# Kernel optimization log

Hardware: AMD Instinct MI355X
Metric: run time of the kernel (lower is better)

The kernel has to match this reference:

```python
import jax, jax.numpy as jnp
import numpy as np

N_ATOMS = 50000
N_EDGES = 1_600_000
N_MOL = 500
HIDDEN = 128
FILTERS = 128
GAUSS = 50
LAYERS = 3
CUTOFF = 10.0
LOG2 = 0.6931471805599453


def ssp(x):
    # ShiftedSoftplus: softplus(x) - log(2)
    return jax.nn.softplus(x) - LOG2


def setup_inputs() -> dict:
    key = jax.random.key(0)
    ks = jax.random.split(key, 24)
    z = jax.random.randint(ks[0], (N_ATOMS,), 0, 100)
    pos = jax.random.uniform(ks[1], (N_ATOMS, 3), jnp.float32) * 5.0  # box keeps d < cutoff
    batch = jnp.sort(jax.random.randint(ks[2], (N_ATOMS,), 0, N_MOL))
    row = jax.random.randint(ks[3], (N_EDGES,), 0, N_ATOMS)
    off = jax.random.randint(ks[4], (N_EDGES,), 1, N_ATOMS)
    col = (row + off) % N_ATOMS  # guarantees row != col (no zero distances)
    edge_index = jnp.stack([row, col])
    def lin(k, fi, fo):
        return jax.random.normal(k, (fi, fo), jnp.float32) * (1.0 / np.sqrt(fi))
    emb = jax.random.normal(ks[5], (100, HIDDEN), jnp.float32)
    mlp1_w = jnp.stack([lin(jax.random.fold_in(ks[6], i), GAUSS, FILTERS) for i in range(LAYERS)])
    mlp1_b = jnp.zeros((LAYERS, FILTERS), jnp.float32)
    mlp2_w = jnp.stack([lin(jax.random.fold_in(ks[7], i), FILTERS, FILTERS) for i in range(LAYERS)])
    mlp2_b = jnp.zeros((LAYERS, FILTERS), jnp.float32)
    lin1_w = jnp.stack([lin(jax.random.fold_in(ks[8], i), HIDDEN, FILTERS) for i in range(LAYERS)])
    lin2_w = jnp.stack([lin(jax.random.fold_in(ks[9], i), FILTERS, HIDDEN) for i in range(LAYERS)])
    lin2_b = jnp.zeros((LAYERS, HIDDEN), jnp.float32)
    int_w = jnp.stack([lin(jax.random.fold_in(ks[10], i), HIDDEN, HIDDEN) for i in range(LAYERS)])
    int_b = jnp.zeros((LAYERS, HIDDEN), jnp.float32)
    out1_w = lin(ks[11], HIDDEN, HIDDEN // 2)
    out1_b = jnp.zeros((HIDDEN // 2,), jnp.float32)
    out2_w = lin(ks[12], HIDDEN // 2, 1)
    out2_b = jnp.zeros((1,), jnp.float32)
    return {"z": z, "pos": pos, "batch": batch, "edge_index": edge_index,
            "emb": emb, "mlp1_w": mlp1_w, "mlp1_b": mlp1_b, "mlp2_w": mlp2_w, "mlp2_b": mlp2_b,
            "lin1_w": lin1_w, "lin2_w": lin2_w, "lin2_b": lin2_b, "int_w": int_w, "int_b": int_b,
            "out1_w": out1_w, "out1_b": out1_b, "out2_w": out2_w, "out2_b": out2_b}


def reference(z, pos, batch, edge_index, emb, mlp1_w, mlp1_b, mlp2_w, mlp2_b,
              lin1_w, lin2_w, lin2_b, int_w, int_b, out1_w, out1_b, out2_w, out2_b):
    row, col = edge_index[0], edge_index[1]  # source j, target i
    d = jnp.linalg.norm(pos[row] - pos[col], axis=-1)  # [E]
    # GaussianSmearing
    offset = jnp.linspace(0.0, CUTOFF, GAUSS)
    coeff = -0.5 / (offset[1] - offset[0]) ** 2
    rbf = jnp.exp(coeff * (d[:, None] - offset[None, :]) ** 2)  # [E, GAUSS]
    # cosine cutoff
    C = 0.5 * (jnp.cos(d * jnp.pi / CUTOFF) + 1.0)  # [E]
    h = emb[z]  # [N, H]
    for l in range(LAYERS):
        W = ssp(rbf @ mlp1_w[l] + mlp1_b[l]) @ mlp2_w[l] + mlp2_b[l]  # [E, F]
        W = W * C[:, None]
        x = h @ lin1_w[l]                 # [N, F]
        msg = x[row] * W                  # gather from source, per-edge filter
        agg = jax.ops.segment_sum(msg, col, num_segments=N_ATOMS)  # scatter-add to targets
        x = agg @ lin2_w[l] + lin2_b[l]
        x = ssp(x)
        x = x @ int_w[l] + int_b[l]
        h = h + x                         # residual
    h = ssp(h @ out1_w + out1_b)
    h = h @ out2_w + out2_b               # [N, 1] per-atom energy
    out = jax.ops.segment_sum(h[:, 0], batch, num_segments=N_MOL)  # 'add' readout
    return out.reshape(-1)
```

## Files before the change

### kernel.cpp

```cpp
#include <hip/hip_runtime.h>
#include <math.h>

#define HID 128
#define NGAUSS 50
#define TBL 2048
#define TBL2 8192
#define DMAX 8.6605f
#define LDX 136
#define PGRID 768

typedef _Float16 h4 __attribute__((ext_vector_type(4)));
typedef _Float16 f16x8 __attribute__((ext_vector_type(8)));
typedef float f32x4 __attribute__((ext_vector_type(4)));

__device__ __forceinline__ float sspf(float x) {
  float ax = fabsf(x);
  return fmaxf(x, 0.0f) + log1pf(expf(-ax)) - 0.69314718055994530942f;
}

__global__ __launch_bounds__(128) void build_table_k(
    const float* __restrict__ w1, const float* __restrict__ b1,
    const float* __restrict__ w2, const float* __restrict__ b2,
    float* __restrict__ tab) {
  int l = blockIdx.x >> 11;
  int ti = blockIdx.x & (TBL - 1);
  int j = threadIdx.x;
  __shared__ float rbf[NGAUSS];
  __shared__ float v1[HID];
  const float step = DMAX / (float)(TBL - 1);
  float d = ti * step;
  if (j < NGAUSS) {
    const float gstep = 10.0f / 49.0f;
    const float gcoeff = -12.005f;
    float diff = d - j * gstep;
    rbf[j] = expf(gcoeff * diff * diff);
  }
  __syncthreads();
  float s = b1[l * HID + j];
  const float* w1p = w1 + l * NGAUSS * HID + j;
  for (int g = 0; g < NGAUSS; g++) s = fmaf(rbf[g], w1p[g * HID], s);
  v1[j] = sspf(s);
  __syncthreads();
  float s2 = b2[l * HID + j];
  const float* w2p = w2 + l * HID * HID + j;
  for (int k = 0; k < HID; k++) s2 = fmaf(v1[k], w2p[k * HID], s2);
  float C = 0.5f * (cosf(d * 0.3141592653589793f) + 1.0f);
  tab[((size_t)l * TBL + ti) * HID + j] = s2 * C;
}

__global__ __launch_bounds__(256) void upsample_k(
    const float* __restrict__ tab, _Float16* __restrict__ tabh) {
  int idx = blockIdx.x * 256 + threadIdx.x;
  if (idx >= 3 * TBL2 * HID) return;
  int ch = idx & 127;
  int i = (idx >> 7) & (TBL2 - 1);
  int l = idx >> 20;
  float t = (float)i * ((float)(TBL - 1) / (float)(TBL2 - 1));
  int i0 = min((int)t, TBL - 2);
  float f = t - (float)i0;
  const float* base = tab + ((size_t)l * TBL + i0) * HID + ch;
  tabh[idx] = (_Float16)fmaf(f, base[HID] - base[0], base[0]);
}

__global__ __launch_bounds__(256) void wswz10_k(
    const float* __restrict__ lin1, const float* __restrict__ lin2,
    const float* __restrict__ intw, const float* __restrict__ out1w,
    _Float16* __restrict__ out) {
  int b = blockIdx.x;
  int t = threadIdx.x;
  if (b < 9) {
    const float* src = (b < 3 ? lin1 : (b < 6 ? lin2 : intw)) + (size_t)(b % 3) * HID * HID;
    _Float16* dst = out + (size_t)b * 16384;
    for (int i = t; i < 16384; i += 256) {
      int j = i & 7;
      int lane = (i >> 3) & 63;
      int kk = (i >> 9) & 3;
      int ntc = i >> 11;
      int n = ntc * 16 + (lane & 15);
      int k = kk * 32 + (lane >> 4) * 8 + j;
      dst[i] = (_Float16)src[k * HID + n];
    }
  } else {
    _Float16* dst = out + (size_t)9 * 16384;
    for (int i = t; i < 8192; i += 256) {
      int j = i & 7;
      int lane = (i >> 3) & 63;
      int kk = (i >> 9) & 3;
      int ntc = i >> 11;
      int n = ntc * 16 + (lane & 15);
      int k = kk * 32 + (lane >> 4) * 8 + j;
      dst[i] = (_Float16)out1w[k * 64 + n];
    }
  }
}

__global__ __launch_bounds__(256) void emb_gather_k(
    const int* __restrict__ z, const float* __restrict__ emb,
    _Float16* __restrict__ h16, int N) {
  int i4 = blockIdx.x * 256 + threadIdx.x;
  if (i4 >= N * 32) return;
  int a = i4 >> 5;
  float4 v = ((const float4*)emb)[z[a] * 32 + (i4 & 31)];
  h4 o;
  o.x = (_Float16)v.x; o.y = (_Float16)v.y;
  o.z = (_Float16)v.z; o.w = (_Float16)v.w;
  ((h4*)h16)[i4] = o;
}

__global__ __launch_bounds__(256) void bcount_k(
    const int* __restrict__ col, int* __restrict__ bcount, int E, int nbuck) {
  __shared__ int hist[1024];
  int t = threadIdx.x;
  int e0 = blockIdx.x * 2048;
  for (int j = t; j < nbuck; j += 256) hist[j] = 0;
  __syncthreads();
#pragma unroll
  for (int u = 0; u < 8; u++) {
    int e = e0 + u * 256 + t;
    if (e < E) atomicAdd(&hist[col[e] >> 6], 1);
  }
  __syncthreads();
  for (int j = t; j < nbuck; j += 256)
    if (hist[j]) atomicAdd(&bcount[j], hist[j]);
}

__global__ __launch_bounds__(256) void bucket_scan_k(
    const int* __restrict__ bcount, int* __restrict__ bstart,
    int* __restrict__ bcur, int nbuck, int* __restrict__ starts, int N) {
  __shared__ int sh[256];
  int t = threadIdx.x;
  int chunk = (nbuck + 255) / 256;
  int b0 = t * chunk;
  int c[8];
  int s = 0;
  for (int j = 0; j < chunk; j++) {
    int idx = b0 + j;
    int v = (idx < nbuck) ? bcount[idx] : 0;
    c[j] = v;
    s += v;
  }
  sh[t] = s;
  __syncthreads();
  for (int o = 1; o < 256; o <<= 1) {
    int v = (t >= o) ? sh[t - o] : 0;
    __syncthreads();
    sh[t] += v;
    __syncthreads();
  }
  int p = (t == 0) ? 0 : sh[t - 1];
  for (int j = 0; j < chunk; j++) {
    int idx = b0 + j;
    if (idx < nbuck) {
      bstart[idx] = p;
      bcur[idx] = p;
      p += c[j];
    }
  }
  if (t == 255) {
    bstart[nbuck] = p;
    starts[N] = p;
  }
}

__global__ __launch_bounds__(256) void scatterA_k(
    const int* __restrict__ row, const int* __restrict__ col,
    const float* __restrict__ pos, int* __restrict__ bcur,
    unsigned long long* __restrict__ tmp, int E, int nbuck) {
  __shared__ int hist[1024];
  __shared__ int base[1024];
  int t = threadIdx.x;
  int e0 = blockIdx.x * 2048;
  for (int j = t; j < nbuck; j += 256) hist[j] = 0;
  __syncthreads();
  int bkt[8];
  int rnk[8];
  unsigned long long key[8];
#pragma unroll
  for (int u = 0; u < 8; u++) {
    int e = e0 + u * 256 + t;
    bkt[u] = -1;
    if (e < E) {
      int r = row[e], c = col[e];
      float dx = pos[r * 3 + 0] - pos[c * 3 + 0];
      float dy = pos[r * 3 + 1] - pos[c * 3 + 1];
      float dz = pos[r * 3 + 2] - pos[c * 3 + 2];
      float d = sqrtf(dx * dx + dy * dy + dz * dz);
      const float inv2 = (float)(TBL2 - 1) / DMAX;
      int q = min((int)(d * inv2 + 0.5f), TBL2 - 1);
      unsigned int pay = ((unsigned int)r << 13) | (unsigned int)q;
      key[u] = ((unsigned long long)pay << 6) | (unsigned long long)(c & 63);
      bkt[u] = c >> 6;
      rnk[u] = atomicAdd(&hist[bkt[u]], 1);
    }
  }
  __syncthreads();
  for (int j = t; j < nbuck; j += 256)
    base[j] = hist[j] ? atomicAdd(&bcur[j], hist[j]) : 0;
  __syncthreads();
#pragma unroll
  for (int u = 0; u < 8; u++)
    if (bkt[u] >= 0) tmp[(size_t)base[bkt[u]] + rnk[u]] = key[u];
}

__global__ __launch_bounds__(256) void scatterB_k(
    const unsigned long long* __restrict__ tmp, const int* __restrict__ bstart,
    int* __restrict__ starts, unsigned int* __restrict__ payload, int N) {
  int j = blockIdx.x;
  int t = threadIdx.x;
  __shared__ int cnt[64];
  __shared__ int cur[64];
  int rs = bstart[j], re = bstart[j + 1];
  if (t < 64) cnt[t] = 0;
  __syncthreads();
  for (int e = rs + t; e < re; e += 256)
    atomicAdd(&cnt[(int)(tmp[e] & 63)], 1);
  __syncthreads();
  if (t < 64) {
    int mine = cnt[t];
    int v = mine;
    for (int o = 1; o < 64; o <<= 1) {
      int u = __shfl_up(v, o, 64);
      if (t >= o) v += u;
    }
    int excl = v - mine;
    int c = j * 64 + t;
    if (c < N) starts[c] = rs + excl;
    cur[t] = rs + excl;
  }
  __syncthreads();
  for (int e = rs + t; e < re; e += 256) {
    unsigned long long k = tmp[e];
    int p = atomicAdd(&cur[(int)(k & 63)], 1);
    payload[p] = (unsigned int)(k >> 6);
  }
}


__global__ __launch_bounds__(256, 4) void lin_p_k(
    const _Float16* __restrict__ in16, const _Float16* __restrict__ Wg,
    _Float16* __restrict__ out16, int N, int ntiles) {
  __shared__ __align__(16) _Float16 Xs[32 * LDX];
  __shared__ __align__(16) _Float16 Ys[32 * LDX];
  int t = threadIdx.x;
  int lane = t & 63, w = t >> 6;
  int g = w & 1, c = w >> 1;
  int mrow = lane & 15, quad = lane >> 4;
  f32x4 zero = {0.f, 0.f, 0.f, 0.f};
  for (int tile = blockIdx.x; tile < ntiles; tile += gridDim.x) {
    int a0 = tile * 32;
#pragma unroll
    for (int p = 0; p < 2; p++) {
      int id = t + p * 256;
      int a = id >> 4, kg = id & 15;
      uint4 v = make_uint4(0, 0, 0, 0);
      if (a0 + a < N) v = ((const uint4*)in16)[(size_t)(a0 + a) * 16 + kg];
      *(uint4*)&Xs[a * LDX + kg * 8] = v;
    }
    __syncthreads();
    f16x8 af[4];
#pragma unroll
    for (int kk = 0; kk < 4; kk++)
      af[kk] = *(const f16x8*)&Xs[(g * 16 + mrow) * LDX + kk * 32 + quad * 8];
    f32x4 acc[4];
#pragma unroll
    for (int i = 0; i < 4; i++) acc[i] = zero;
#pragma unroll
    for (int kk = 0; kk < 4; kk++) {
#pragma unroll
      for (int nt = 0; nt < 4; nt++) {
        f16x8 bf = *(const f16x8*)(Wg + ((((c * 4 + nt) * 4 + kk) << 9) + lane * 8));
        acc[nt] = __builtin_amdgcn_mfma_f32_16x16x32_f16(af[kk], bf, acc[nt], 0, 0, 0);
      }
    }
#pragma unroll
    for (int nt = 0; nt < 4; nt++) {
      int colv = c * 64 + nt * 16 + mrow;
#pragma unroll
      for (int r = 0; r < 4; r++)
        Ys[(g * 16 + quad * 4 + r) * LDX + colv] = (_Float16)acc[nt][r];
    }
    __syncthreads();
#pragma unroll
    for (int p = 0; p < 2; p++) {
      int id = t + p * 256;
      int a = id >> 4, kg = id & 15;
      if (a0 + a < N)
        ((uint4*)out16)[(size_t)(a0 + a) * 16 + kg] = *(uint4*)&Ys[a * LDX + kg * 8];
    }
  }
}

__global__ __launch_bounds__(256, 4) void ssp_p_k(
    const _Float16* __restrict__ agg16, const _Float16* __restrict__ Wg,
    const float* __restrict__ bias, _Float16* __restrict__ y16, int N, int ntiles) {
  __shared__ __align__(16) _Float16 Xs[32 * LDX];
  __shared__ __align__(16) _Float16 Ys[32 * LDX];
  int t = threadIdx.x;
  int lane = t & 63, w = t >> 6;
  int g = w & 1, c = w >> 1;
  int mrow = lane & 15, quad = lane >> 4;
  float br[4];
#pragma unroll
  for (int nt = 0; nt < 4; nt++) br[nt] = bias[c * 64 + nt * 16 + mrow];
  f32x4 zero = {0.f, 0.f, 0.f, 0.f};
  for (int tile = blockIdx.x; tile < ntiles; tile += gridDim.x) {
    int a0 = tile * 32;
#pragma unroll
    for (int p = 0; p < 2; p++) {
      int id = t + p * 256;
      int a = id >> 4, kg = id & 15;
      uint4 v = make_uint4(0, 0, 0, 0);
      if (a0 + a < N) v = ((const uint4*)agg16)[(size_t)(a0 + a) * 16 + kg];
      *(uint4*)&Xs[a * LDX + kg * 8] = v;
    }
    __syncthreads();
    f16x8 af[4];
#pragma unroll
    for (int kk = 0; kk < 4; kk++)
      af[kk] = *(const f16x8*)&Xs[(g * 16 + mrow) * LDX + kk * 32 + quad * 8];
    f32x4 acc[4];
#pragma unroll
    for (int i = 0; i < 4; i++) acc[i] = zero;
#pragma unroll
    for (int kk = 0; kk < 4; kk++) {
#pragma unroll
      for (int nt = 0; nt < 4; nt++) {
        f16x8 bf = *(const f16x8*)(Wg + ((((c * 4 + nt) * 4 + kk) << 9) + lane * 8));
        acc[nt] = __builtin_amdgcn_mfma_f32_16x16x32_f16(af[kk], bf, acc[nt], 0, 0, 0);
      }
    }
#pragma unroll
    for (int nt = 0; nt < 4; nt++) {
      int colv = c * 64 + nt * 16 + mrow;
#pragma unroll
      for (int r = 0; r < 4; r++)
        Ys[(g * 16 + quad * 4 + r) * LDX + colv] = (_Float16)sspf(acc[nt][r] + br[nt]);
    }
    __syncthreads();
#pragma unroll
    for (int p = 0; p < 2; p++) {
      int id = t + p * 256;
      int a = id >> 4, kg = id & 15;
      if (a0 + a < N)
        ((uint4*)y16)[(size_t)(a0 + a) * 16 + kg] = *(uint4*)&Ys[a * LDX + kg * 8];
    }
  }
}

__global__ __launch_bounds__(256, 4) void res_p_k(
    const _Float16* __restrict__ y16, const _Float16* __restrict__ Wg,
    const float* __restrict__ bias, _Float16* __restrict__ h16, int N, int ntiles) {
  __shared__ __align__(16) _Float16 Xs[32 * LDX];
  __shared__ __align__(16) _Float16 Ys[32 * LDX];
  int t = threadIdx.x;
  int lane = t & 63, w = t >> 6;
  int g = w & 1, c = w >> 1;
  int mrow = lane & 15, quad = lane >> 4;
  float br[4];
#pragma unroll
  for (int nt = 0; nt < 4; nt++) br[nt] = bias[c * 64 + nt * 16 + mrow];
  f32x4 zero = {0.f, 0.f, 0.f, 0.f};
  for (int tile = blockIdx.x; tile < ntiles; tile += gridDim.x) {
    int a0 = tile * 32;
#pragma unroll
    for (int p = 0; p < 2; p++) {
      int id = t + p * 256;
      int a = id >> 4, kg = id & 15;
      uint4 v = make_uint4(0, 0, 0, 0);
      if (a0 + a < N) v = ((const uint4*)y16)[(size_t)(a0 + a) * 16 + kg];
      *(uint4*)&Xs[a * LDX + kg * 8] = v;
    }
    __syncthreads();
    f16x8 af[4];
#pragma unroll
    for (int kk = 0; kk < 4; kk++)
      af[kk] = *(const f16x8*)&Xs[(g * 16 + mrow) * LDX + kk * 32 + quad * 8];
    f32x4 acc[4];
#pragma unroll
    for (int i = 0; i < 4; i++) acc[i] = zero;
#pragma unroll
    for (int kk = 0; kk < 4; kk++) {
#pragma unroll
      for (int nt = 0; nt < 4; nt++) {
        f16x8 bf = *(const f16x8*)(Wg + ((((c * 4 + nt) * 4 + kk) << 9) + lane * 8));
        acc[nt] = __builtin_amdgcn_mfma_f32_16x16x32_f16(af[kk], bf, acc[nt], 0, 0, 0);
      }
    }
#pragma unroll
    for (int nt = 0; nt < 4; nt++) {
      int colv = c * 64 + nt * 16 + mrow;
#pragma unroll
      for (int r = 0; r < 4; r++)
        Ys[(g * 16 + quad * 4 + r) * LDX + colv] = (_Float16)(acc[nt][r] + br[nt]);
    }
    __syncthreads();
#pragma unroll
    for (int p = 0; p < 2; p++) {
      int id = t + p * 256;
      int a = id >> 4, kg = id & 15;
      if (a0 + a < N) {
        f16x8 hv = *(const f16x8*)&((const uint4*)h16)[(size_t)(a0 + a) * 16 + kg];
        f16x8 yv = *(f16x8*)&Ys[a * LDX + kg * 8];
        f16x8 o;
#pragma unroll
        for (int j = 0; j < 8; j++) o[j] = (_Float16)((float)hv[j] + (float)yv[j]);
        ((uint4*)h16)[(size_t)(a0 + a) * 16 + kg] = *(uint4*)&o;
      }
    }
  }
}

__global__ __launch_bounds__(256, 4) void energy_p_k(
    const _Float16* __restrict__ h16, const _Float16* __restrict__ Wg,
    const float* __restrict__ o1b, const float* __restrict__ o2w,
    const float* __restrict__ o2b, const int* __restrict__ batch,
    float* __restrict__ out, int N, int ntiles) {
  __shared__ __align__(16) _Float16 Xs[32 * LDX];
  __shared__ float ebuf[32];
  __shared__ int bat[32];
  int t = threadIdx.x;
  int lane = t & 63, w = t >> 6;
  int g = w & 1, c = w >> 1;
  int mrow = lane & 15, quad = lane >> 4;
  float br[2], wr[2];
#pragma unroll
  for (int nt = 0; nt < 2; nt++) {
    int colv = c * 32 + nt * 16 + mrow;
    br[nt] = o1b[colv];
    wr[nt] = o2w[colv];
  }
  float o2b0 = o2b[0];
  if (t < 32) ebuf[t] = 0.f;
  __syncthreads();
  f32x4 zero = {0.f, 0.f, 0.f, 0.f};
  for (int tile = blockIdx.x; tile < ntiles; tile += gridDim.x) {
    int a0 = tile * 32;
#pragma unroll
    for (int p = 0; p < 2; p++) {
      int id = t + p * 256;
      int a = id >> 4, kg = id & 15;
      uint4 v = make_uint4(0, 0, 0, 0);
      if (a0 + a < N) v = ((const uint4*)h16)[(size_t)(a0 + a) * 16 + kg];
      *(uint4*)&Xs[a * LDX + kg * 8] = v;
    }
    if (t < 32) bat[t] = (a0 + t < N) ? batch[a0 + t] : -1;
    __syncthreads();
    f16x8 af[4];
#pragma unroll
    for (int kk = 0; kk < 4; kk++)
      af[kk] = *(const f16x8*)&Xs[(g * 16 + mrow) * LDX + kk * 32 + quad * 8];
    f32x4 acc[2];
    acc[0] = zero; acc[1] = zero;
#pragma unroll
    for (int kk = 0; kk < 4; kk++) {
#pragma unroll
      for (int nt = 0; nt < 2; nt++) {
        f16x8 bf = *(const f16x8*)(Wg + ((((c * 2 + nt) * 4 + kk) << 9) + lane * 8));
        acc[nt] = __builtin_amdgcn_mfma_f32_16x16x32_f16(af[kk], bf, acc[nt], 0, 0, 0);
      }
    }
    float ss[4] = {0.f, 0.f, 0.f, 0.f};
#pragma unroll
    for (int nt = 0; nt < 2; nt++)
#pragma unroll
      for (int r = 0; r < 4; r++) ss[r] += sspf(acc[nt][r] + br[nt]) * wr[nt];
#pragma unroll
    for (int r = 0; r < 4; r++) {
      ss[r] += __shfl_xor(ss[r], 1);
      ss[r] += __shfl_xor(ss[r], 2);
      ss[r] += __shfl_xor(ss[r], 4);
      ss[r] += __shfl_xor(ss[r], 8);
      if (mrow == 0) atomicAdd(&ebuf[g * 16 + quad * 4 + r], ss[r]);
    }
    __syncthreads();
    if (t == 0) {
      float acs = 0.f;
      int pm = -1;
      for (int i = 0; i < 32; i++) {
        int m = bat[i];
        float e = ebuf[i];
        ebuf[i] = 0.f;
        if (m < 0) break;
        if (m != pm) {
          if (pm >= 0) atomicAdd(&out[pm], acs);
          acs = 0.f;
          pm = m;
        }
        acs += e + o2b0;
      }
      if (pm >= 0) atomicAdd(&out[pm], acs);
    }
  }
}

__global__ __launch_bounds__(256) void aggregate_k(
    const int* __restrict__ starts, const unsigned int* __restrict__ payload,
    const _Float16* __restrict__ x16, const _Float16* __restrict__ tabh,
    _Float16* __restrict__ agg16, int N) {
  int a = blockIdx.x * 4 + (threadIdx.x >> 6);
  if (a >= N) return;
  int lane = threadIdx.x & 63;
  int half = lane >> 5;
  int sl = lane & 31;
  int s = starts[a], e_end = starts[a + 1];
  float4 accf = make_float4(0.f, 0.f, 0.f, 0.f);
  const h4 z4 = {(_Float16)0.f, (_Float16)0.f, (_Float16)0.f, (_Float16)0.f};
  auto do_edge = [&](unsigned int p, h4& acc) {
    int tq = (int)(p & 8191u);
    int r = (int)(p >> 13);
    h4 tw = *(const h4*)&tabh[(size_t)tq * HID + sl * 4];
    h4 xr = *(const h4*)&x16[(size_t)r * HID + sl * 4];
    acc += tw * xr;
  };
  auto flush = [&](h4 a0, h4 a1) {
    accf.x += (float)a0.x + (float)a1.x;
    accf.y += (float)a0.y + (float)a1.y;
    accf.z += (float)a0.z + (float)a1.z;
    accf.w += (float)a0.w + (float)a1.w;
  };
  int i = s;
  for (; i + 16 <= e_end; i += 16) {
    h4 a0 = z4, a1 = z4;
    do_edge(payload[i + half], a0);
    do_edge(payload[i + 2 + half], a1);
    do_edge(payload[i + 4 + half], a0);
    do_edge(payload[i + 6 + half], a1);
    do_edge(payload[i + 8 + half], a0);
    do_edge(payload[i + 10 + half], a1);
    do_edge(payload[i + 12 + half], a0);
    do_edge(payload[i + 14 + half], a1);
    flush(a0, a1);
  }
  {
    h4 a0 = z4, a1 = z4;
    int k = 0;
    for (; i + 2 <= e_end; i += 2, k++) do_edge(payload[i + half], (k & 1) ? a1 : a0);
    if (i < e_end && half == 0) do_edge(payload[i], a0);
    flush(a0, a1);
  }
  accf.x += __shfl_xor(accf.x, 32);
  accf.y += __shfl_xor(accf.y, 32);
  accf.z += __shfl_xor(accf.z, 32);
  accf.w += __shfl_xor(accf.w, 32);
  if (half == 0) {
    h4 o;
    o.x = (_Float16)accf.x; o.y = (_Float16)accf.y;
    o.z = (_Float16)accf.z; o.w = (_Float16)accf.w;
    *(h4*)&agg16[(size_t)a * HID + sl * 4] = o;
  }
}

extern "C" void kernel_launch(void* const* d_in, const int* in_sizes, int n_in,
                              void* d_out, int out_size, void* d_ws, size_t ws_size,
                              hipStream_t stream) {
  const int* z = (const int*)d_in[0];
  const float* pos = (const float*)d_in[1];
  const int* batch = (const int*)d_in[2];
  const int* eidx = (const int*)d_in[3];
  const float* emb = (const float*)d_in[4];
  const float* mlp1_w = (const float*)d_in[5];
  const float* mlp1_b = (const float*)d_in[6];
  const float* mlp2_w = (const float*)d_in[7];
  const float* mlp2_b = (const float*)d_in[8];
  const float* lin1_w = (const float*)d_in[9];
  const float* lin2_w = (const float*)d_in[10];
  const float* lin2_b = (const float*)d_in[11];
  const float* int_w = (const float*)d_in[12];
  const float* int_b = (const float*)d_in[13];
  const float* out1_w = (const float*)d_in[14];
  const float* out1_b = (const float*)d_in[15];
  const float* out2_w = (const float*)d_in[16];
  const float* out2_b = (const float*)d_in[17];
  float* out = (float*)d_out;

  const int N = in_sizes[0];
  const int E = in_sizes[3] / 2;
  const int* row = eidx;
  const int* col = eidx + E;
  const int nbuck = (N + 63) / 64;
  const int ntiles = (N + 31) / 32;

  char* ws = (char*)d_ws;
  size_t off = 0;
  auto alloc = [&](size_t bytes) -> void* {
    void* p = ws + off;
    off = (off + bytes + 255) & ~(size_t)255;
    return p;
  };
  _Float16* h16 = (_Float16*)alloc((size_t)N * HID * 2);
  _Float16* x16 = (_Float16*)alloc((size_t)N * HID * 2);
  size_t agg_bytes = (size_t)N * HID * 2;
  size_t tmp_bytes = (size_t)E * 8 + 16;
  void* agg_union = alloc(agg_bytes > tmp_bytes ? agg_bytes : tmp_bytes);
  _Float16* agg16 = (_Float16*)agg_union;
  unsigned long long* tmp = (unsigned long long*)agg_union;
  unsigned int* payload = (unsigned int*)alloc((size_t)E * 4 + 16);
  int* starts = (int*)alloc((size_t)(N + 1) * 4);
  int* bcount = (int*)alloc((size_t)nbuck * 4);
  int* bstart = (int*)alloc((size_t)(nbuck + 1) * 4);
  int* bcur = (int*)alloc((size_t)nbuck * 4);
  float* tab = (float*)alloc((size_t)3 * TBL * HID * 4);
  _Float16* tabh = (_Float16*)alloc((size_t)3 * TBL2 * HID * 2);
  _Float16* Wsw = (_Float16*)alloc((size_t)10 * 16384 * 2);
  (void)ws_size;

  hipMemsetAsync(bcount, 0, (size_t)nbuck * 4, stream);
  hipMemsetAsync(out, 0, (size_t)out_size * 4, stream);

  build_table_k<<<3 * TBL, 128, 0, stream>>>(mlp1_w, mlp1_b, mlp2_w, mlp2_b, tab);
  upsample_k<<<(3 * TBL2 * HID + 255) / 256, 256, 0, stream>>>(tab, tabh);
  wswz10_k<<<10, 256, 0, stream>>>(lin1_w, lin2_w, int_w, out1_w, Wsw);
  emb_gather_k<<<(N * 32 + 255) / 256, 256, 0, stream>>>(z, emb, h16, N);
  bcount_k<<<(E + 2047) / 2048, 256, 0, stream>>>(col, bcount, E, nbuck);
  bucket_scan_k<<<1, 256, 0, stream>>>(bcount, bstart, bcur, nbuck, starts, N);
  scatterA_k<<<(E + 2047) / 2048, 256, 0, stream>>>(row, col, pos, bcur, tmp, E, nbuck);
  scatterB_k<<<nbuck, 256, 0, stream>>>(tmp, bstart, starts, payload, N);

  int pg = PGRID < ntiles ? PGRID : ntiles;
  for (int l = 0; l < 3; l++) {
    lin_p_k<<<pg, 256, 0, stream>>>(h16, Wsw + (size_t)l * 16384, x16, N, ntiles);
    aggregate_k<<<(N + 3) / 4, 256, 0, stream>>>(starts, payload, x16,
                                                 tabh + (size_t)l * TBL2 * HID, agg16, N);
    ssp_p_k<<<pg, 256, 0, stream>>>(agg16, Wsw + (size_t)(3 + l) * 16384,
                                    lin2_b + (size_t)l * HID, x16, N, ntiles);
    res_p_k<<<pg, 256, 0, stream>>>(x16, Wsw + (size_t)(6 + l) * 16384,
                                    int_b + (size_t)l * HID, h16, N, ntiles);
  }
  energy_p_k<<<pg, 256, 0, stream>>>(h16, Wsw + (size_t)9 * 16384, out1_b, out2_w,
                                     out2_b, batch, out, N, ntiles);
}
```

Before: 555.3 us.

## Fuse ssp and residual GEMMs per layer; batch gathers in edge aggregation

Merges the lin2+shifted-softplus kernel and the interaction+residual kernel into one kernel, so the intermediate tile stays in shared memory and is fed straight into the second MFMA GEMM instead of round-tripping through global memory. This removes one launch per layer and an N×128 fp16 write and read. Separately, the aggregation loop now loads all eight payloads first, then issues all table and feature gathers before accumulating into four fp16 partial sums, which exposes more memory-level parallelism at the cost of more registers.

```diff
diff --git a/kernel.cpp b/kernel.cpp
--- a/kernel.cpp
+++ b/kernel.cpp
@@ -290,18 +290,22 @@
   }
 }
 
-__global__ __launch_bounds__(256, 4) void ssp_p_k(
-    const _Float16* __restrict__ agg16, const _Float16* __restrict__ Wg,
-    const float* __restrict__ bias, _Float16* __restrict__ y16, int N, int ntiles) {
+__global__ __launch_bounds__(256, 4) void ssp_res_p_k(
+    const _Float16* __restrict__ agg16, const _Float16* __restrict__ W2g,
+    const float* __restrict__ b2, const _Float16* __restrict__ W3g,
+    const float* __restrict__ b3, _Float16* __restrict__ h16, int N, int ntiles) {
   __shared__ __align__(16) _Float16 Xs[32 * LDX];
   __shared__ __align__(16) _Float16 Ys[32 * LDX];
   int t = threadIdx.x;
   int lane = t & 63, w = t >> 6;
   int g = w & 1, c = w >> 1;
   int mrow = lane & 15, quad = lane >> 4;
-  float br[4];
-#pragma unroll
-  for (int nt = 0; nt < 4; nt++) br[nt] = bias[c * 64 + nt * 16 + mrow];
+  float br2[4], br3[4];
+#pragma unroll
+  for (int nt = 0; nt < 4; nt++) {
+    br2[nt] = b2[c * 64 + nt * 16 + mrow];
+    br3[nt] = b3[c * 64 + nt * 16 + mrow];
+  }
   f32x4 zero = {0.f, 0.f, 0.f, 0.f};
   for (int tile = blockIdx.x; tile < ntiles; tile += gridDim.x) {
     int a0 = tile * 32;
@@ -325,7 +329,7 @@
     for (int kk = 0; kk < 4; kk++) {
 #pragma unroll
       for (int nt = 0; nt < 4; nt++) {
-        f16x8 bf = *(const f16x8*)(Wg + ((((c * 4 + nt) * 4 + kk) << 9) + lane * 8));
+        f16x8 bf = *(const f16x8*)(W2g + ((((c * 4 + nt) * 4 + kk) << 9) + lane * 8));
         acc[nt] = __builtin_amdgcn_mfma_f32_16x16x32_f16(af[kk], bf, acc[nt], 0, 0, 0);
       }
     }
@@ -334,55 +338,20 @@
       int colv = c * 64 + nt * 16 + mrow;
 #pragma unroll
       for (int r = 0; r < 4; r++)
-        Ys[(g * 16 + quad * 4 + r) * LDX + colv] = (_Float16)sspf(acc[nt][r] + br[nt]);
-    }
-    __syncthreads();
-#pragma unroll
-    for (int p = 0; p < 2; p++) {
-      int id = t + p * 256;
-      int a = id >> 4, kg = id & 15;
-      if (a0 + a < N)
-        ((uint4*)y16)[(size_t)(a0 + a) * 16 + kg] = *(uint4*)&Ys[a * LDX + kg * 8];
-    }
-  }
-}
-
-__global__ __launch_bounds__(256, 4) void res_p_k(
-    const _Float16* __restrict__ y16, const _Float16* __restrict__ Wg,
-    const float* __restrict__ bias, _Float16* __restrict__ h16, int N, int ntiles) {
-  __shared__ __align__(16) _Float16 Xs[32 * LDX];
-  __shared__ __align__(16) _Float16 Ys[32 * LDX];
-  int t = threadIdx.x;
-  int lane = t & 63, w = t >> 6;
-  int g = w & 1, c = w >> 1;
-  int mrow = lane & 15, quad = lane >> 4;
-  float br[4];
-#pragma unroll
-  for (int nt = 0; nt < 4; nt++) br[nt] = bias[c * 64 + nt * 16 + mrow];
-  f32x4 zero = {0.f, 0.f, 0.f, 0.f};
-  for (int tile = blockIdx.x; tile < ntiles; tile += gridDim.x) {
-    int a0 = tile * 32;
-#pragma unroll
-    for (int p = 0; p < 2; p++) {
-      int id = t + p * 256;
-      int a = id >> 4, kg = id & 15;
-      uint4 v = make_uint4(0, 0, 0, 0);
-      if (a0 + a < N) v = ((const uint4*)y16)[(size_t)(a0 + a) * 16 + kg];
-      *(uint4*)&Xs[a * LDX + kg * 8] = v;
-    }
-    __syncthreads();
-    f16x8 af[4];
+        Ys[(g * 16 + quad * 4 + r) * LDX + colv] = (_Float16)sspf(acc[nt][r] + br2[nt]);
+    }
+    __syncthreads();
 #pragma unroll
     for (int kk = 0; kk < 4; kk++)
-      af[kk] = *(const f16x8*)&Xs[(g * 16 + mrow) * LDX + kk * 32 + quad * 8];
-    f32x4 acc[4];
+      af[kk] = *(const f16x8*)&Ys[(g * 16 + mrow) * LDX + kk * 32 + quad * 8];
+    __syncthreads();
 #pragma unroll
     for (int i = 0; i < 4; i++) acc[i] = zero;
 #pragma unroll
     for (int kk = 0; kk < 4; kk++) {
 #pragma unroll
       for (int nt = 0; nt < 4; nt++) {
-        f16x8 bf = *(const f16x8*)(Wg + ((((c * 4 + nt) * 4 + kk) << 9) + lane * 8));
+        f16x8 bf = *(const f16x8*)(W3g + ((((c * 4 + nt) * 4 + kk) << 9) + lane * 8));
         acc[nt] = __builtin_amdgcn_mfma_f32_16x16x32_f16(af[kk], bf, acc[nt], 0, 0, 0);
       }
     }
@@ -391,7 +360,7 @@
       int colv = c * 64 + nt * 16 + mrow;
 #pragma unroll
       for (int r = 0; r < 4; r++)
-        Ys[(g * 16 + quad * 4 + r) * LDX + colv] = (_Float16)(acc[nt][r] + br[nt]);
+        Ys[(g * 16 + quad * 4 + r) * LDX + colv] = (_Float16)(acc[nt][r] + br3[nt]);
     }
     __syncthreads();
 #pragma unroll
@@ -505,38 +474,58 @@
   int s = starts[a], e_end = starts[a + 1];
   float4 accf = make_float4(0.f, 0.f, 0.f, 0.f);
   const h4 z4 = {(_Float16)0.f, (_Float16)0.f, (_Float16)0.f, (_Float16)0.f};
-  auto do_edge = [&](unsigned int p, h4& acc) {
-    int tq = (int)(p & 8191u);
-    int r = (int)(p >> 13);
-    h4 tw = *(const h4*)&tabh[(size_t)tq * HID + sl * 4];
-    h4 xr = *(const h4*)&x16[(size_t)r * HID + sl * 4];
-    acc += tw * xr;
-  };
-  auto flush = [&](h4 a0, h4 a1) {
-    accf.x += (float)a0.x + (float)a1.x;
-    accf.y += (float)a0.y + (float)a1.y;
-    accf.z += (float)a0.z + (float)a1.z;
-    accf.w += (float)a0.w + (float)a1.w;
-  };
   int i = s;
   for (; i + 16 <= e_end; i += 16) {
-    h4 a0 = z4, a1 = z4;
-    do_edge(payload[i + half], a0);
-    do_edge(payload[i + 2 + half], a1);
-    do_edge(payload[i + 4 + half], a0);
-    do_edge(payload[i + 6 + half], a1);
-    do_edge(payload[i + 8 + half], a0);
-    do_edge(payload[i + 10 + half], a1);
-    do_edge(payload[i + 12 + half], a0);
-    do_edge(payload[i + 14 + half], a1);
-    flush(a0, a1);
+    unsigned int p[8];
+#pragma unroll
+    for (int u = 0; u < 8; u++) p[u] = payload[i + 2 * u + half];
+    h4 tw[8], xr[8];
+#pragma unroll
+    for (int u = 0; u < 8; u++) {
+      int tq = (int)(p[u] & 8191u);
+      int r = (int)(p[u] >> 13);
+      tw[u] = *(const h4*)&tabh[(size_t)tq * HID + sl * 4];
+      xr[u] = *(const h4*)&x16[(size_t)r * HID + sl * 4];
+    }
+    h4 a0 = z4, a1 = z4, a2 = z4, a3 = z4;
+    a0 += tw[0] * xr[0];
+    a1 += tw[1] * xr[1];
+    a2 += tw[2] * xr[2];
+    a3 += tw[3] * xr[3];
+    a0 += tw[4] * xr[4];
+    a1 += tw[5] * xr[5];
+    a2 += tw[6] * xr[6];
+    a3 += tw[7] * xr[7];
+    h4 b0 = a0 + a1, b1 = a2 + a3;
+    accf.x += (float)b0.x + (float)b1.x;
+    accf.y += (float)b0.y + (float)b1.y;
+    accf.z += (float)b0.z + (float)b1.z;
+    accf.w += (float)b0.w + (float)b1.w;
   }
   {
     h4 a0 = z4, a1 = z4;
     int k = 0;
-    for (; i + 2 <= e_end; i += 2, k++) do_edge(payload[i + half], (k & 1) ? a1 : a0);
-    if (i < e_end && half == 0) do_edge(payload[i], a0);
-    flush(a0, a1);
+    for (; i + 2 <= e_end; i += 2, k++) {
+      unsigned int p = payload[i + half];
+      int tq = (int)(p & 8191u);
+      int r = (int)(p >> 13);
+      h4 tw = *(const h4*)&tabh[(size_t)tq * HID + sl * 4];
+      h4 xr = *(const h4*)&x16[(size_t)r * HID + sl * 4];
+      if (k & 1) a1 += tw * xr; else a0 += tw * xr;
+    }
+    if (i < e_end && half == 0) {
+      unsigned int p = payload[i];
+      int tq = (int)(p & 8191u);
+      int r = (int)(p >> 13);
+      h4 tw = *(const h4*)&tabh[(size_t)tq * HID + sl * 4];
+      h4 xr = *(const h4*)&x16[(size_t)r * HID + sl * 4];
+      a0 += tw * xr;
+    }
+    h4 b0 = a0 + a1;
+    accf.x += (float)b0.x;
+    accf.y += (float)b0.y;
+    accf.z += (float)b0.z;
+    accf.w += (float)b0.w;
   }
   accf.x += __shfl_xor(accf.x, 32);
   accf.y += __shfl_xor(accf.y, 32);
@@ -621,10 +610,10 @@
     lin_p_k<<<pg, 256, 0, stream>>>(h16, Wsw + (size_t)l * 16384, x16, N, ntiles);
     aggregate_k<<<(N + 3) / 4, 256, 0, stream>>>(starts, payload, x16,
                                                  tabh + (size_t)l * TBL2 * HID, agg16, N);
-    ssp_p_k<<<pg, 256, 0, stream>>>(agg16, Wsw + (size_t)(3 + l) * 16384,
-                                    lin2_b + (size_t)l * HID, x16, N, ntiles);
-    res_p_k<<<pg, 256, 0, stream>>>(x16, Wsw + (size_t)(6 + l) * 16384,
-                                    int_b + (size_t)l * HID, h16, N, ntiles);
+    ssp_res_p_k<<<pg, 256, 0, stream>>>(agg16, Wsw + (size_t)(3 + l) * 16384,
+                                        lin2_b + (size_t)l * HID,
+                                        Wsw + (size_t)(6 + l) * 16384,
+                                        int_b + (size_t)l * HID, h16, N, ntiles);
   }
   energy_p_k<<<pg, 256, 0, stream>>>(h16, Wsw + (size_t)9 * 16384, out1_b, out2_w,
                                      out2_b, batch, out, N, ntiles);
```

Measured after the change: 570.6 us. +2.8%, slower.

## Split node features and filter table into 32-channel planes for aggregation

Applied to the files above, without the earlier changes.

Stores x16, agg16 and the filter table as four 32-channel planes, so each aggregation block gathers only 64-byte slices from one plane. Blocks are interleaved across planes to keep each plane's working set cache-resident, and each wave handles eight edges at once with a shuffle reduction. The upsampled filter table resolution is also halved to shrink its footprint. In exchange, edge payloads are re-read once per plane and the coarser table interpolation adds approximation error.

```diff
diff --git a/kernel.cpp b/kernel.cpp
--- a/kernel.cpp
+++ b/kernel.cpp
@@ -4,7 +4,7 @@
 #define HID 128
 #define NGAUSS 50
 #define TBL 2048
-#define TBL2 8192
+#define TBL2 4096
 #define DMAX 8.6605f
 #define LDX 136
 #define PGRID 768
@@ -49,17 +49,19 @@
 }
 
 __global__ __launch_bounds__(256) void upsample_k(
-    const float* __restrict__ tab, _Float16* __restrict__ tabh) {
+    const float* __restrict__ tab, _Float16* __restrict__ tabhb) {
   int idx = blockIdx.x * 256 + threadIdx.x;
   if (idx >= 3 * TBL2 * HID) return;
   int ch = idx & 127;
   int i = (idx >> 7) & (TBL2 - 1);
-  int l = idx >> 20;
+  int l = idx / (TBL2 * HID);
   float t = (float)i * ((float)(TBL - 1) / (float)(TBL2 - 1));
   int i0 = min((int)t, TBL - 2);
   float f = t - (float)i0;
   const float* base = tab + ((size_t)l * TBL + i0) * HID + ch;
-  tabh[idx] = (_Float16)fmaf(f, base[HID] - base[0], base[0]);
+  int p = ch >> 5, c32 = ch & 31;
+  tabhb[(((size_t)(l * 4 + p) * TBL2 + i) << 5) + c32] =
+      (_Float16)fmaf(f, base[HID] - base[0], base[0]);
 }
 
 __global__ __launch_bounds__(256) void wswz10_k(
@@ -238,7 +240,7 @@
 
 __global__ __launch_bounds__(256, 4) void lin_p_k(
     const _Float16* __restrict__ in16, const _Float16* __restrict__ Wg,
-    _Float16* __restrict__ out16, int N, int ntiles) {
+    _Float16* __restrict__ x16b, int N, int ntiles) {
   __shared__ __align__(16) _Float16 Xs[32 * LDX];
   __shared__ __align__(16) _Float16 Ys[32 * LDX];
   int t = threadIdx.x;
@@ -285,13 +287,14 @@
       int id = t + p * 256;
       int a = id >> 4, kg = id & 15;
       if (a0 + a < N)
-        ((uint4*)out16)[(size_t)(a0 + a) * 16 + kg] = *(uint4*)&Ys[a * LDX + kg * 8];
+        ((uint4*)x16b)[((size_t)(kg >> 2) * N + (a0 + a)) * 4 + (kg & 3)] =
+            *(uint4*)&Ys[a * LDX + kg * 8];
     }
   }
 }
 
 __global__ __launch_bounds__(256, 4) void ssp_p_k(
-    const _Float16* __restrict__ agg16, const _Float16* __restrict__ Wg,
+    const _Float16* __restrict__ agg16b, const _Float16* __restrict__ Wg,
     const float* __restrict__ bias, _Float16* __restrict__ y16, int N, int ntiles) {
   __shared__ __align__(16) _Float16 Xs[32 * LDX];
   __shared__ __align__(16) _Float16 Ys[32 * LDX];
@@ -310,7 +313,8 @@
       int id = t + p * 256;
       int a = id >> 4, kg = id & 15;
       uint4 v = make_uint4(0, 0, 0, 0);
-      if (a0 + a < N) v = ((const uint4*)agg16)[(size_t)(a0 + a) * 16 + kg];
+      if (a0 + a < N)
+        v = ((const uint4*)agg16b)[((size_t)(kg >> 2) * N + (a0 + a)) * 4 + (kg & 3)];
       *(uint4*)&Xs[a * LDX + kg * 8] = v;
     }
     __syncthreads();
@@ -495,58 +499,75 @@
 
 __global__ __launch_bounds__(256) void aggregate_k(
     const int* __restrict__ starts, const unsigned int* __restrict__ payload,
-    const _Float16* __restrict__ x16, const _Float16* __restrict__ tabh,
-    _Float16* __restrict__ agg16, int N) {
-  int a = blockIdx.x * 4 + (threadIdx.x >> 6);
+    const _Float16* __restrict__ x16b, const _Float16* __restrict__ tabhb,
+    _Float16* __restrict__ agg16b, int N, int nbp) {
+  int b = blockIdx.x;
+  int p = (b & 7) >> 1;
+  int k = (b >> 3) * 2 + (b & 1);
+  if (k >= nbp) return;
+  int w = threadIdx.x >> 6;
+  int a = k * 4 + w;
   if (a >= N) return;
   int lane = threadIdx.x & 63;
-  int half = lane >> 5;
-  int sl = lane & 31;
+  int e_sub = lane >> 3;
+  int cg = lane & 7;
+  const _Float16* xp = x16b + ((size_t)p * N << 5) + cg * 4;
+  const _Float16* tp = tabhb + ((size_t)p * TBL2 << 5) + cg * 4;
   int s = starts[a], e_end = starts[a + 1];
   float4 accf = make_float4(0.f, 0.f, 0.f, 0.f);
   const h4 z4 = {(_Float16)0.f, (_Float16)0.f, (_Float16)0.f, (_Float16)0.f};
-  auto do_edge = [&](unsigned int p, h4& acc) {
-    int tq = (int)(p & 8191u);
-    int r = (int)(p >> 13);
-    h4 tw = *(const h4*)&tabh[(size_t)tq * HID + sl * 4];
-    h4 xr = *(const h4*)&x16[(size_t)r * HID + sl * 4];
-    acc += tw * xr;
-  };
-  auto flush = [&](h4 a0, h4 a1) {
-    accf.x += (float)a0.x + (float)a1.x;
-    accf.y += (float)a0.y + (float)a1.y;
-    accf.z += (float)a0.z + (float)a1.z;
-    accf.w += (float)a0.w + (float)a1.w;
-  };
   int i = s;
   for (; i + 16 <= e_end; i += 16) {
-    h4 a0 = z4, a1 = z4;
-    do_edge(payload[i + half], a0);
-    do_edge(payload[i + 2 + half], a1);
-    do_edge(payload[i + 4 + half], a0);
-    do_edge(payload[i + 6 + half], a1);
-    do_edge(payload[i + 8 + half], a0);
-    do_edge(payload[i + 10 + half], a1);
-    do_edge(payload[i + 12 + half], a0);
-    do_edge(payload[i + 14 + half], a1);
-    flush(a0, a1);
+    unsigned int p0 = payload[i + e_sub];
+    unsigned int p1 = payload[i + 8 + e_sub];
+    int tq0 = (int)(p0 & 8191u), r0 = (int)(p0 >> 13);
+    int tq1 = (int)(p1 & 8191u), r1 = (int)(p1 >> 13);
+    h4 tw0 = *(const h4*)(tp + ((size_t)tq0 << 5));
+    h4 xr0 = *(const h4*)(xp + ((size_t)r0 << 5));
+    h4 tw1 = *(const h4*)(tp + ((size_t)tq1 << 5));
+    h4 xr1 = *(const h4*)(xp + ((size_t)r1 << 5));
+    h4 acc16 = z4;
+    acc16 += tw0 * xr0;
+    acc16 += tw1 * xr1;
+    accf.x += (float)acc16.x;
+    accf.y += (float)acc16.y;
+    accf.z += (float)acc16.z;
+    accf.w += (float)acc16.w;
   }
   {
-    h4 a0 = z4, a1 = z4;
-    int k = 0;
-    for (; i + 2 <= e_end; i += 2, k++) do_edge(payload[i + half], (k & 1) ? a1 : a0);
-    if (i < e_end && half == 0) do_edge(payload[i], a0);
-    flush(a0, a1);
-  }
+    h4 acc16 = z4;
+    for (; i < e_end; i += 8) {
+      int e = i + e_sub;
+      if (e < e_end) {
+        unsigned int pp = payload[e];
+        int tq = (int)(pp & 8191u), r = (int)(pp >> 13);
+        h4 tw = *(const h4*)(tp + ((size_t)tq << 5));
+        h4 xr = *(const h4*)(xp + ((size_t)r << 5));
+        acc16 += tw * xr;
+      }
+    }
+    accf.x += (float)acc16.x;
+    accf.y += (float)acc16.y;
+    accf.z += (float)acc16.z;
+    accf.w += (float)acc16.w;
+  }
+  accf.x += __shfl_xor(accf.x, 8);
+  accf.y += __shfl_xor(accf.y, 8);
+  accf.z += __shfl_xor(accf.z, 8);
+  accf.w += __shfl_xor(accf.w, 8);
+  accf.x += __shfl_xor(accf.x, 16);
+  accf.y += __shfl_xor(accf.y, 16);
+  accf.z += __shfl_xor(accf.z, 16);
+  accf.w += __shfl_xor(accf.w, 16);
   accf.x += __shfl_xor(accf.x, 32);
   accf.y += __shfl_xor(accf.y, 32);
   accf.z += __shfl_xor(accf.z, 32);
   accf.w += __shfl_xor(accf.w, 32);
-  if (half == 0) {
+  if (e_sub == 0) {
     h4 o;
     o.x = (_Float16)accf.x; o.y = (_Float16)accf.y;
     o.z = (_Float16)accf.z; o.w = (_Float16)accf.w;
-    *(h4*)&agg16[(size_t)a * HID + sl * 4] = o;
+    *(h4*)(agg16b + (((size_t)p * N + a) << 5) + cg * 4) = o;
   }
 }
 
@@ -600,7 +621,7 @@
   int* bstart = (int*)alloc((size_t)(nbuck + 1) * 4);
   int* bcur = (int*)alloc((size_t)nbuck * 4);
   float* tab = (float*)alloc((size_t)3 * TBL * HID * 4);
-  _Float16* tabh = (_Float16*)alloc((size_t)3 * TBL2 * HID * 2);
+  _Float16* tabhb = (_Float16*)alloc((size_t)3 * TBL2 * HID * 2);
   _Float16* Wsw = (_Float16*)alloc((size_t)10 * 16384 * 2);
   (void)ws_size;
 
@@ -608,7 +629,7 @@
   hipMemsetAsync(out, 0, (size_t)out_size * 4, stream);
 
   build_table_k<<<3 * TBL, 128, 0, stream>>>(mlp1_w, mlp1_b, mlp2_w, mlp2_b, tab);
-  upsample_k<<<(3 * TBL2 * HID + 255) / 256, 256, 0, stream>>>(tab, tabh);
+  upsample_k<<<(3 * TBL2 * HID + 255) / 256, 256, 0, stream>>>(tab, tabhb);
   wswz10_k<<<10, 256, 0, stream>>>(lin1_w, lin2_w, int_w, out1_w, Wsw);
   emb_gather_k<<<(N * 32 + 255) / 256, 256, 0, stream>>>(z, emb, h16, N);
   bcount_k<<<(E + 2047) / 2048, 256, 0, stream>>>(col, bcount, E, nbuck);
@@ -617,10 +638,13 @@
   scatterB_k<<<nbuck, 256, 0, stream>>>(tmp, bstart, starts, payload, N);
 
   int pg = PGRID < ntiles ? PGRID : ntiles;
+  const int nbp = (N + 3) / 4;
+  const int agg_grid = ((nbp + 1) / 2) * 8;
   for (int l = 0; l < 3; l++) {
     lin_p_k<<<pg, 256, 0, stream>>>(h16, Wsw + (size_t)l * 16384, x16, N, ntiles);
-    aggregate_k<<<(N + 3) / 4, 256, 0, stream>>>(starts, payload, x16,
-                                                 tabh + (size_t)l * TBL2 * HID, agg16, N);
+    aggregate_k<<<agg_grid, 256, 0, stream>>>(starts, payload, x16,
+                                              tabhb + (size_t)l * 4 * TBL2 * 32,
+                                              agg16, N, nbp);
     ssp_p_k<<<pg, 256, 0, stream>>>(agg16, Wsw + (size_t)(3 + l) * 16384,
                                     lin2_b + (size_t)l * HID, x16, N, ntiles);
     res_p_k<<<pg, 256, 0, stream>>>(x16, Wsw + (size_t)(6 + l) * 16384,
```

Result: slower. 631.9 us (+13.8%).
